# Optimization experiments

Measured on AMD Instinct MI355X. Metric: run time of the kernel, lower is better.

The kernel has to match this reference:

```python
import jax, jax.numpy as jnp
import numpy as np

N = 4096          # number of graph nodes
N_IN = 128        # number of input nodes
N_OUT = 32        # number of output nodes
MASK_DENSITY = 0.01


def setup_inputs() -> dict:
    key = jax.random.key(0)
    k_obs, k_w, k_a = jax.random.split(key, 3)
    obs = jax.random.normal(k_obs, (N_IN,), dtype=jnp.float32)
    W = jax.random.normal(k_w, (N, N), dtype=jnp.float32)
    # adjacency mask: sparse 0/1 matrix like nx.adjacency_matrix
    A = (jax.random.uniform(k_a, (N, N)) < MASK_DENSITY).astype(jnp.float32)
    input_ids = jnp.arange(N_IN, dtype=jnp.int32)            # input-typed nodes
    output_ids = jnp.arange(N - N_OUT, N, dtype=jnp.int32)   # output-typed nodes
    return {"obs": obs, "W": W, "A": A, "input_ids": input_ids,
            "output_ids": output_ids, "depth": 4}


def reference(obs, W, A, input_ids, output_ids, depth):
    # masked weights: abs(W) * A (has_bias=False path)
    Wm = jnp.abs(W) * A
    WmT = Wm.T  # hoist transpose out of the recurrence
    x0 = jnp.zeros((N,), dtype=W.dtype)

    def step(x, _):
        x = x.at[input_ids].set(obs)      # clamp input nodes to obs
        x = jnp.tanh(WmT @ x)             # one message-passing step
        return x, None

    x, _ = jax.lax.scan(step, x0, None, length=depth)
    return x[output_ids]
```

## Files before the change

### kernel.cpp

```cpp
#include <hip/hip_runtime.h>


#define NN 4096
#define N_IN 128
#define N_OUT_C 32
#define CAP 96
#define LCAP 32
#define DEPTH_FIXED 4

typedef float floatx4 __attribute__((ext_vector_type(4)));

__global__ __launch_bounds__(256)
void extract_kernel(const floatx4* __restrict__ W4,
                    const floatx4* __restrict__ A4,
                    int* __restrict__ cnt,
                    uint2* __restrict__ ent) {
    __shared__ int   lcnt[32];
    __shared__ int   gbase[32];
    __shared__ uint2 lent[32][LCAP];

    const int strip   = blockIdx.x >> 3;
    const int colBase = strip * 32;
    const int rowBase = (blockIdx.x & 7) * 512;
    const int t  = threadIdx.x;
    const int tq = t & 7;
    const int tr = t >> 3;

    if (t < 32) lcnt[t] = 0;
    __syncthreads();

    const int cq = (colBase >> 2) + tq;
    for (int r0 = 0; r0 < 512; r0 += 128) {
        floatx4 a[4];
        int rows[4];
#pragma unroll
        for (int u = 0; u < 4; ++u) {
            rows[u] = rowBase + r0 + u * 32 + tr;
            a[u] = A4[(size_t)rows[u] * (NN / 4) + cq];
        }
#pragma unroll
        for (int u = 0; u < 4; ++u) {
            floatx4 av = a[u];
            if (av.x == 0.f && av.y == 0.f && av.z == 0.f && av.w == 0.f) continue;
            floatx4 wv = W4[(size_t)rows[u] * (NN / 4) + cq];
            float aa[4] = {av.x, av.y, av.z, av.w};
            float ww[4] = {wv.x, wv.y, wv.z, wv.w};
#pragma unroll
            for (int q = 0; q < 4; ++q) {
                if (aa[q] != 0.f) {
                    int c = tq * 4 + q;
                    int pos = atomicAdd(&lcnt[c], 1);
                    if (pos < LCAP)
                        lent[c][pos] = make_uint2((unsigned)rows[u],
                                                  __float_as_uint(fabsf(ww[q])));
                }
            }
        }
    }
    __syncthreads();

    if (t < 32) {
        int lc = lcnt[t]; if (lc > LCAP) lc = LCAP;
        lcnt[t]  = lc;
        gbase[t] = atomicAdd(&cnt[colBase + t], lc);
    }
    __syncthreads();

    {
        int c  = t >> 3;
        int p0 = t & 7;
        int lc = lcnt[c];
        int gb = gbase[c];
        for (int p = p0; p < lc; p += 8) {
            int g = gb + p;
            if (g < CAP)
                ent[(size_t)(colBase + c) * CAP + g] = lent[c][p];
        }
    }
}

__global__ __launch_bounds__(256)
void step_kernel(const int* __restrict__ cnt,
                 const uint2* __restrict__ ent,
                 const float* __restrict__ xin,
                 const float* __restrict__ obs,
                 float* __restrict__ xout,
                 int firstStep, int clampOut) {
    int t   = blockIdx.x * 256 + threadIdx.x;
    int col = t >> 4;
    int sub = t & 15;

    int c = cnt[col]; if (c > CAP) c = CAP;

    float sum = 0.f;
    for (int e = sub; e < c; e += 16) {
        uint2 ev = ent[(size_t)col * CAP + e];
        int j = (int)ev.x;
        float xv = firstStep ? ((j < N_IN) ? obs[j] : 0.f) : xin[j];
        sum += __uint_as_float(ev.y) * xv;
    }
    sum += __shfl_xor(sum, 1, 64);
    sum += __shfl_xor(sum, 2, 64);
    sum += __shfl_xor(sum, 4, 64);
    sum += __shfl_xor(sum, 8, 64);

    if (sub == 0) {
        float v = tanhf(sum);
        if (clampOut && col < N_IN) v = obs[col];
        xout[col] = v;
    }
}

__global__ __launch_bounds__(256)
void final_kernel(const int* __restrict__ cnt,
                  const uint2* __restrict__ ent,
                  const float* __restrict__ xin,
                  const int* __restrict__ out_ids,
                  float* __restrict__ out, int n_out) {
    int t   = blockIdx.x * 256 + threadIdx.x;
    int g   = t >> 4;
    int sub = t & 15;
    if (g >= n_out) return;

    int i = out_ids[g];
    int c = cnt[i]; if (c > CAP) c = CAP;

    float sum = 0.f;
    for (int e = sub; e < c; e += 16) {
        uint2 ev = ent[(size_t)i * CAP + e];
        sum += __uint_as_float(ev.y) * xin[ev.x];
    }
    sum += __shfl_xor(sum, 1, 64);
    sum += __shfl_xor(sum, 2, 64);
    sum += __shfl_xor(sum, 4, 64);
    sum += __shfl_xor(sum, 8, 64);

    if (sub == 0) out[g] = tanhf(sum);
}

extern "C" void kernel_launch(void* const* d_in, const int* in_sizes, int n_in,
                              void* d_out, int out_size, void* d_ws, size_t ws_size,
                              hipStream_t stream) {
    const float* obs        = (const float*)d_in[0];
    const float* W          = (const float*)d_in[1];
    const float* A          = (const float*)d_in[2];
    const int*   output_ids = (const int*)d_in[4];
    float*       out        = (float*)d_out;

    char*  ws  = (char*)d_ws;
    int*   cnt = (int*)ws;
    uint2* ent = (uint2*)(ws + NN * sizeof(int));
    float* xA  = (float*)((char*)ent + (size_t)NN * CAP * sizeof(uint2));
    float* xB  = xA + NN;

    (void)hipMemsetAsync(cnt, 0, NN * sizeof(int), stream);

    extract_kernel<<<128 * 8, 256, 0, stream>>>(
        (const floatx4*)W, (const floatx4*)A, cnt, ent);

    step_kernel<<<256, 256, 0, stream>>>(cnt, ent, nullptr, obs, xA, 1, 1);
    step_kernel<<<256, 256, 0, stream>>>(cnt, ent, xA,      obs, xB, 0, 1);
    step_kernel<<<256, 256, 0, stream>>>(cnt, ent, xB,      obs, xA, 0, 1);

    int n_out = (out_size < N_OUT_C) ? out_size : N_OUT_C;
    final_kernel<<<(n_out * 16 + 255) / 256, 256, 0, stream>>>(
        cnt, ent, xA, output_ids, out, n_out);
}
```

Measured before the change: 42.10 us.

## Defer W gathers to the write-out phase and issue all A loads up front

The extract kernel now loads all 16 A vectors per thread before scanning, where it used to load them in groups of 4, so more loads are in flight at once. It records only row indices (as 16-bit values) in shared memory during the scan. The W values are read as single floats during the final write-out, and only for entries that are actually kept, instead of reading a full float4 of W whenever any lane in the vector is nonzero. This cuts W traffic and shared memory use, at the cost of more registers and scattered scalar loads of W in the write-out loop.

```diff
diff --git a/kernel.cpp b/kernel.cpp
--- a/kernel.cpp
+++ b/kernel.cpp
@@ -11,13 +11,13 @@
 typedef float floatx4 __attribute__((ext_vector_type(4)));
 
 __global__ __launch_bounds__(256)
-void extract_kernel(const floatx4* __restrict__ W4,
+void extract_kernel(const float* __restrict__ W,
                     const floatx4* __restrict__ A4,
                     int* __restrict__ cnt,
                     uint2* __restrict__ ent) {
-    __shared__ int   lcnt[32];
-    __shared__ int   gbase[32];
-    __shared__ uint2 lent[32][LCAP];
+    __shared__ unsigned short lrow[32][LCAP];
+    __shared__ int lcnt[32];
+    __shared__ int gbase[32];
 
     const int strip   = blockIdx.x >> 3;
     const int colBase = strip * 32;
@@ -30,30 +30,24 @@
     __syncthreads();
 
     const int cq = (colBase >> 2) + tq;
-    for (int r0 = 0; r0 < 512; r0 += 128) {
-        floatx4 a[4];
-        int rows[4];
+    floatx4 a[16];
 #pragma unroll
-        for (int u = 0; u < 4; ++u) {
-            rows[u] = rowBase + r0 + u * 32 + tr;
-            a[u] = A4[(size_t)rows[u] * (NN / 4) + cq];
-        }
+    for (int u = 0; u < 16; ++u) {
+        int row = rowBase + u * 32 + tr;
+        a[u] = A4[(size_t)row * (NN / 4) + cq];
+    }
 #pragma unroll
-        for (int u = 0; u < 4; ++u) {
-            floatx4 av = a[u];
-            if (av.x == 0.f && av.y == 0.f && av.z == 0.f && av.w == 0.f) continue;
-            floatx4 wv = W4[(size_t)rows[u] * (NN / 4) + cq];
-            float aa[4] = {av.x, av.y, av.z, av.w};
-            float ww[4] = {wv.x, wv.y, wv.z, wv.w};
+    for (int u = 0; u < 16; ++u) {
+        floatx4 av = a[u];
+        if (av.x == 0.f && av.y == 0.f && av.z == 0.f && av.w == 0.f) continue;
+        int row = rowBase + u * 32 + tr;
+        float aa[4] = {av.x, av.y, av.z, av.w};
 #pragma unroll
-            for (int q = 0; q < 4; ++q) {
-                if (aa[q] != 0.f) {
-                    int c = tq * 4 + q;
-                    int pos = atomicAdd(&lcnt[c], 1);
-                    if (pos < LCAP)
-                        lent[c][pos] = make_uint2((unsigned)rows[u],
-                                                  __float_as_uint(fabsf(ww[q])));
-                }
+        for (int q = 0; q < 4; ++q) {
+            if (aa[q] != 0.f) {
+                int c = tq * 4 + q;
+                int pos = atomicAdd(&lcnt[c], 1);
+                if (pos < LCAP) lrow[c][pos] = (unsigned short)row;
             }
         }
     }
@@ -67,14 +61,16 @@
     __syncthreads();
 
     {
-        int c  = t >> 3;
-        int p0 = t & 7;
+        int c  = t & 31;
         int lc = lcnt[c];
         int gb = gbase[c];
-        for (int p = p0; p < lc; p += 8) {
+        for (int p = t >> 5; p < lc; p += 8) {
+            int row = (int)lrow[c][p];
+            float w = W[(size_t)row * NN + colBase + c];
             int g = gb + p;
             if (g < CAP)
-                ent[(size_t)(colBase + c) * CAP + g] = lent[c][p];
+                ent[(size_t)(colBase + c) * CAP + g] =
+                    make_uint2((unsigned)row, __float_as_uint(fabsf(w)));
         }
     }
 }
@@ -156,7 +152,7 @@
     (void)hipMemsetAsync(cnt, 0, NN * sizeof(int), stream);
 
     extract_kernel<<<128 * 8, 256, 0, stream>>>(
-        (const floatx4*)W, (const floatx4*)A, cnt, ent);
+        W, (const floatx4*)A, cnt, ent);
 
     step_kernel<<<256, 256, 0, stream>>>(cnt, ent, nullptr, obs, xA, 1, 1);
     step_kernel<<<256, 256, 0, stream>>>(cnt, ent, xA,      obs, xB, 0, 1);
```

New measurement: 42.53 us. Within noise of the previous version (+1.0%).
